# Optimization experiments

Hardware: AMD Instinct MI355X
Metric: run time of the kernel (lower is better)

The kernel has to match this reference:

```python
import jax, jax.numpy as jnp
import numpy as np

N_NODES = 30522
HID = 768
N_EDGES = 488352
B, S = 4, 512
L = 12  # transformer_layers
C = 100  # num classes in pos-neg codebook graph


def setup_inputs() -> dict:
    key = jax.random.key(0)
    ks = jax.random.split(key, 20)
    inp = {}
    inp["word_embs"] = jax.random.normal(ks[0], (N_NODES, HID), dtype=jnp.float32)
    inp["input_ids"] = jax.random.randint(ks[1], (B, S), 0, N_NODES + 1)  # N_NODES = padding row
    inp["class_ids"] = jax.random.randint(ks[2], (B, S), 0, C + 1)
    inp["mask"] = jax.random.randint(ks[3], (B, S, 1), 0, 2).astype(bool)
    inp["co_edge_index"] = jax.random.randint(ks[4], (2, N_EDGES), 0, N_NODES)
    inp["co_edge_weight"] = jax.random.uniform(ks[5], (N_EDGES,), dtype=jnp.float32)
    inp["re_edge_index"] = jax.random.randint(ks[6], (2, N_EDGES), 0, N_NODES)
    inp["re_edge_weight"] = jax.random.uniform(ks[7], (N_EDGES,), dtype=jnp.float32)
    pn_graph = jax.random.uniform(ks[8], (C + 1, N_NODES), dtype=jnp.float32) * 0.01
    inp["pn_graph"] = pn_graph.at[-1].set(0.0)  # padding row of zeros
    sc = 0.02
    inp["co_W"] = jax.random.normal(ks[9], (3, HID, HID), dtype=jnp.float32) * sc
    inp["co_b"] = jnp.zeros((3, HID), jnp.float32)
    inp["re_W"] = jax.random.normal(ks[10], (3, HID, HID), dtype=jnp.float32) * sc
    inp["re_b"] = jnp.zeros((3, HID), jnp.float32)
    inp["pn_W"] = jax.random.normal(ks[11], (HID, HID), dtype=jnp.float32) * sc  # [out,in] 1x1 conv
    inp["pn_b"] = jnp.zeros((HID,), jnp.float32)
    # zero_convs are zero-initialized in the original; use small random so math is non-trivial
    inp["zero_w"] = jax.random.normal(ks[12], (L, HID, HID), dtype=jnp.float32) * sc
    inp["zero_b"] = jnp.zeros((L, HID), jnp.float32)
    inp["zero_w_pos"] = jax.random.normal(ks[13], (L, HID, HID), dtype=jnp.float32) * sc
    inp["zero_b_pos"] = jnp.zeros((L, HID), jnp.float32)
    return inp


def _gcn_layer(x, src, dst, ew, W, b, n):
    # PyG GCNConv: add self-loops (weight 1), symmetric normalization
    deg = jax.ops.segment_sum(ew, dst, num_segments=n) + 1.0
    dinv = jnp.where(deg > 0, jax.lax.rsqrt(deg), 0.0)
    norm = dinv[src] * ew * dinv[dst]  # [E]
    h = x @ W  # [n, H]
    agg = jax.ops.segment_sum(norm[:, None] * h[src], dst, num_segments=n)
    agg = agg + h * (dinv * dinv)[:, None]  # self-loop contribution
    return agg + b


def _gcn_stack(x, edge_index, ew, Ws, bs, ids):
    src, dst = edge_index[0], edge_index[1]
    n = x.shape[0]
    h = x
    acc = None
    for i in range(3):
        h = jax.nn.relu(_gcn_layer(h, src, dst, ew, Ws[i], bs[i], n))
        pad = jnp.concatenate([h, jnp.zeros((1, h.shape[-1]), h.dtype)], axis=0)
        g = pad[ids]  # [B, S, H] gather with padding row
        acc = g if acc is None else acc + g
    return acc / 3.0


def _zero_conv_layers(tok, w, b):
    # 1x1 conv over hidden channels for each of L layers: [B,S,H] x [L,O,H] -> [L,B,S,O]
    return jnp.einsum("bsh,loh->lbso", tok, w) + b[:, None, None, :]


def reference(word_embs, input_ids, class_ids, mask,
              co_edge_index, co_edge_weight, re_edge_index, re_edge_weight,
              pn_graph, co_W, co_b, re_W, re_b, pn_W, pn_b,
              zero_w, zero_b, zero_w_pos, zero_b_pos):
    Bq, Sq = input_ids.shape
    H = word_embs.shape[-1]
    Lq = zero_w.shape[0]
    inv_mask = (~mask).astype(word_embs.dtype)  # [B,S,1]
    zero_pad = jnp.zeros((Lq, Bq, 1, H), word_embs.dtype)

    co = _gcn_stack(word_embs, co_edge_index, co_edge_weight, co_W, co_b, input_ids)  # [B,S,H]
    re = _gcn_stack(word_embs, re_edge_index, re_edge_weight, re_W, re_b, input_ids)

    # NOTE: original uses self.zero_convs (not a separate set) for BOTH co and re
    co_l = _zero_conv_layers(co, zero_w, zero_b) * inv_mask[None]
    re_l = _zero_conv_layers(re, zero_w, zero_b) * inv_mask[None]
    co_l = jnp.concatenate([zero_pad, co_l], axis=2)  # [L,B,S+1,H]
    re_l = jnp.concatenate([zero_pad, re_l], axis=2)

    # PosNegCodebook: 1x1 conv on codebook, then dense-graph matmul, gathered by class
    cb = word_embs @ pn_W.T + pn_b  # [N, H]
    pn = (pn_graph @ cb)[class_ids]  # [B,S,H] (same math as graph[class_ids] @ cb)
    pn_l = _zero_conv_layers(pn, zero_w_pos, zero_b_pos)
    pn_l = jnp.concatenate([zero_pad, pn_l], axis=2)

    return (co_l, re_l, pn_l)
```

## Files before the change

### kernel.cpp

```cpp
#include <hip/hip_runtime.h>
#include <stdint.h>

typedef unsigned int u32;
typedef unsigned short u16;
typedef __attribute__((ext_vector_type(8))) short short8;
typedef __attribute__((ext_vector_type(4))) float f32x4;

#define N_NODESC 30522
#define HIDC 768
#define NEC 488352
#define TOKM 2048
#define LLAY 12
#define NCLS 101
#define M_PAD 30720
#define ZNC (LLAY*HIDC)
#define OUT_SET (LLAY*4*513*HIDC)
#define PN_KCHUNK 512
#define NBLK 120
#define NN1 (N_NODESC+1)
#define G8_LDS 131072

__device__ __forceinline__ float bl(u32 u){ return __uint_as_float(u<<16); }
__device__ __forceinline__ float bh(u32 u){ return __uint_as_float(u & 0xffff0000u); }
__device__ __forceinline__ u32 f2b1(float f){ u32 x=__float_as_uint(f); return (x + 0x7fffu + ((x>>16)&1u))>>16; }
__device__ __forceinline__ u32 pack2(float a, float b){ return f2b1(a) | (f2b1(b)<<16); }

__device__ __forceinline__ void mfma16(f32x4& d, short8 a, short8 b){
  asm volatile("v_mfma_f32_16x16x32_bf16 %0, %1, %2, %0" : "+v"(d) : "v"(a), "v"(b));
}
__device__ __forceinline__ void async16(const void* g, void* l){
  __builtin_amdgcn_global_load_lds((const __attribute__((address_space(1))) u32*)g,
                                   (__attribute__((address_space(3))) u32*)l, 16, 0, 0);
}

__global__ void k_invmask(const void* __restrict__ mask, float* __restrict__ invm){
  __shared__ int s_byte, s_flt;
  int t = threadIdx.x;
  const unsigned char* mb = (const unsigned char*)mask;
  const u32* mw = (const u32*)mask;
  int lb=0, lf=0;
  for(int i=t;i<2048;i+=256) if((i&3)!=0 && mb[i]!=0) lb=1;
  for(int i=t;i<512;i+=256) if(mw[i]==0x3F800000u) lf=1;
  if(t==0){ s_byte=0; s_flt=0; }
  __syncthreads();
  if(lb) s_byte=1;
  if(lf) s_flt=1;
  __syncthreads();
  int mode = s_flt ? 2 : (s_byte ? 1 : 0);
  for(int p=t;p<2048;p+=256){
    int mv = (mode==1) ? (int)mb[p] : (int)(mw[p]!=0u);
    invm[p] = mv ? 0.f : 1.f;
  }
}

__global__ void k_needed(const int* __restrict__ ids, u32* __restrict__ needed){
  int p = blockIdx.x*256 + threadIdx.x;
  if(p < TOKM){ int id = ids[p]; if(id < N_NODESC) needed[id] = 1u; }
}

__global__ void k_need1_init(const u32* __restrict__ needed, u32* __restrict__ need1){
  int v = blockIdx.x*256 + threadIdx.x;
  if(v < N_NODESC){ u32 x = needed[v]; need1[v] = x; need1[N_NODESC + v] = x; }
}
__global__ void k_need_expand(const int* __restrict__ coei, const int* __restrict__ reei,
                              const u32* __restrict__ needed, u32* __restrict__ need1){
  int g = blockIdx.y;
  const int* ei = g ? reei : coei;
  int e = blockIdx.x*256 + threadIdx.x;
  if(e < NEC){
    int d = ei[NEC+e];
    if(needed[d]) need1[(size_t)g*N_NODESC + ei[e]] = 1u;
  }
}

__global__ void k_conv(const float* __restrict__ src, u16* __restrict__ dst, int ndw){
  int i = blockIdx.x*256 + threadIdx.x;
  if(i < ndw) ((u32*)dst)[i] = pack2(src[2*i], src[2*i+1]);
}
__global__ void k_conv_pad(const float* __restrict__ src, u16* __restrict__ dst, int srcRows, int padRows){
  int i = blockIdx.x*256 + threadIdx.x;
  if(i >= padRows*384) return;
  int row = i/384; int c2 = (i - row*384)*2;
  float lo=0.f, hi=0.f;
  if(row < srcRows){ const float* s = src + (size_t)row*HIDC + c2; lo=s[0]; hi=s[1]; }
  ((u32*)dst)[i] = pack2(lo, hi);
}
__global__ void k_pnb(const float* __restrict__ png, u16* __restrict__ pnb){
  int i = blockIdx.x*256 + threadIdx.x;
  if(i >= 128*(M_PAD/2)) return;
  int row = i/(M_PAD/2); int k2 = (i - row*(M_PAD/2))*2;
  float lo=0.f, hi=0.f;
  if(row < NCLS){
    const float* s = png + (size_t)row*N_NODESC;
    if(k2 < N_NODESC) lo = s[k2];
    if(k2+1 < N_NODESC) hi = s[k2+1];
  }
  ((u32*)pnb)[i] = pack2(lo, hi);
}
__global__ void k_transposeW2(const float* __restrict__ coW, const float* __restrict__ reW,
                              u16* __restrict__ Wt2){
  int g = blockIdx.y;
  int i = blockIdx.x*256 + threadIdx.x;
  if(i >= 3*HIDC*384) return;
  const float* W = g ? reW : coW;
  int mat = i/(HIDC*384); int rem = i - mat*HIDC*384;
  int n = rem/384; int kd = rem - n*384;
  const float* Wm = W + (size_t)mat*HIDC*HIDC;
  float lo = Wm[(size_t)(2*kd)*HIDC + n];
  float hi = Wm[(size_t)(2*kd+1)*HIDC + n];
  ((u32*)Wt2)[(size_t)g*3*HIDC*384 + (size_t)mat*HIDC*384 + (size_t)n*384 + kd] = pack2(lo, hi);
}

__global__ void k_degcnt2(const int* __restrict__ coei, const int* __restrict__ reei,
                          const float* __restrict__ coew, const float* __restrict__ reew,
                          float* __restrict__ deg2, int* __restrict__ cnt2){
  int g = blockIdx.y;
  const int* ei = g ? reei : coei;
  const float* ew = g ? reew : coew;
  int e = blockIdx.x*256 + threadIdx.x;
  if(e < NEC){ int d = ei[NEC+e]; atomicAdd(&deg2[(size_t)g*N_NODESC + d], ew[e]); atomicAdd(&cnt2[(size_t)g*N_NODESC + d], 1); }
}
__global__ void k_dinv2(const float* __restrict__ deg2, float* __restrict__ dinvA, float* __restrict__ dinvB){
  int g = blockIdx.y;
  int v = blockIdx.x*256 + threadIdx.x;
  if(v < N_NODESC){
    float d = deg2[(size_t)g*N_NODESC + v] + 1.f;
    dinvA[(size_t)g*N_NODESC + v] = rsqrtf(d);
    dinvB[(size_t)g*N_NODESC + v] = 1.f/d;
  }
}
__global__ void k_scan1(const int* __restrict__ cnt2, int* __restrict__ part2){
  __shared__ int wt[4];
  int g = blockIdx.y, b = blockIdx.x, t = threadIdx.x;
  int lane = t & 63, w = t >> 6;
  int i = b*256 + t;
  int v = (i < N_NODESC) ? cnt2[(size_t)g*N_NODESC + i] : 0;
  int x = v;
  #pragma unroll
  for(int off=1; off<64; off<<=1){ int y = __shfl_up(x, off); if(lane>=off) x += y; }
  if(lane==63) wt[w] = x;
  __syncthreads();
  if(t==0) part2[g*NBLK + b] = wt[0]+wt[1]+wt[2]+wt[3];
}
__global__ void k_scan2(int* __restrict__ part2, int* __restrict__ rp2){
  __shared__ int w0tot;
  int g = blockIdx.x, t = threadIdx.x;
  int lane = t & 63, w = t >> 6;
  int v = (t < NBLK) ? part2[g*NBLK + t] : 0;
  int x = v;
  #pragma unroll
  for(int off=1; off<64; off<<=1){ int y = __shfl_up(x, off); if(lane>=off) x += y; }
  if(w==0 && lane==63) w0tot = x;
  __syncthreads();
  int incl = x + (w ? w0tot : 0);
  int excl = incl - v;
  if(t < NBLK) part2[g*NBLK + t] = excl;
  if(t == 127) rp2[(size_t)g*NN1 + N_NODESC] = incl;
}
__global__ void k_scan3(const int* __restrict__ cnt2, const int* __restrict__ part2,
                        int* __restrict__ rp2, int* __restrict__ cur2){
  __shared__ int wt[4];
  int g = blockIdx.y, b = blockIdx.x, t = threadIdx.x;
  int lane = t & 63, w = t >> 6;
  int i = b*256 + t;
  int v = (i < N_NODESC) ? cnt2[(size_t)g*N_NODESC + i] : 0;
  int x = v;
  #pragma unroll
  for(int off=1; off<64; off<<=1){ int y = __shfl_up(x, off); if(lane>=off) x += y; }
  if(lane==63) wt[w] = x;
  __syncthreads();
  int wpre = 0;
  #pragma unroll
  for(int j=0;j<4;j++) if(j<w) wpre += wt[j];
  int excl = x - v + wpre + part2[g*NBLK + b];
  if(i < N_NODESC){ rp2[(size_t)g*NN1 + i] = excl; cur2[(size_t)g*N_NODESC + i] = excl; }
}
__global__ void k_scatter2(const int* __restrict__ coei, const int* __restrict__ reei,
                           const float* __restrict__ coew, const float* __restrict__ reew,
                           const float* __restrict__ dinvA, int* __restrict__ cur2,
                           float2* __restrict__ emeta){
  int g = blockIdx.y;
  const int* ei = g ? reei : coei;
  const float* ew = g ? reew : coew;
  int e = blockIdx.x*256 + threadIdx.x;
  if(e < NEC){
    int s = ei[e], d = ei[NEC+e];
    int pos = atomicAdd(&cur2[(size_t)g*N_NODESC + d], 1);
    float nrm = dinvA[(size_t)g*N_NODESC + s]*ew[e]*dinvA[(size_t)g*N_NODESC + d];
    emeta[(size_t)g*NEC + pos] = make_float2(__int_as_float(s), nrm);
  }
}

__global__ __launch_bounds__(256)
void k_spmm(const u16* __restrict__ hW, const int* __restrict__ rp,
            const float2* __restrict__ emeta, const float* __restrict__ dinv2,
            const float* __restrict__ bias, u16* __restrict__ hout,
            const u32* __restrict__ needed){
  int v = blockIdx.x*4 + (threadIdx.x>>6);
  if(v >= N_NODESC) return;
  if(needed && !needed[v]) return;
  int lane = threadIdx.x & 63;
  const u32* H = (const u32*)hW;
  float acc[12];
  #pragma unroll
  for(int q=0;q<12;q++) acc[q]=0.f;
  int e0 = rp[v], e1 = rp[v+1];
  int e = e0;
  for(; e+4<=e1; e+=4){
    float2 m0=emeta[e], m1=emeta[e+1], m2=emeta[e+2], m3=emeta[e+3];
    const u32* r0 = H + (size_t)__float_as_int(m0.x)*384 + lane;
    const u32* r1 = H + (size_t)__float_as_int(m1.x)*384 + lane;
    const u32* r2 = H + (size_t)__float_as_int(m2.x)*384 + lane;
    const u32* r3 = H + (size_t)__float_as_int(m3.x)*384 + lane;
    u32 u0[6],u1[6],u2[6],u3[6];
    #pragma unroll
    for(int q=0;q<6;q++){ u0[q]=r0[q*64]; u1[q]=r1[q*64]; u2[q]=r2[q*64]; u3[q]=r3[q*64]; }
    #pragma unroll
    for(int q=0;q<6;q++){
      acc[2*q]   += m0.y*bl(u0[q]) + m1.y*bl(u1[q]) + m2.y*bl(u2[q]) + m3.y*bl(u3[q]);
      acc[2*q+1] += m0.y*bh(u0[q]) + m1.y*bh(u1[q]) + m2.y*bh(u2[q]) + m3.y*bh(u3[q]);
    }
  }
  for(; e<e1; ++e){
    float2 mm = emeta[e];
    const u32* r = H + (size_t)__float_as_int(mm.x)*384 + lane;
    #pragma unroll
    for(int q=0;q<6;q++){ u32 u = r[q*64]; acc[2*q] += mm.y*bl(u); acc[2*q+1] += mm.y*bh(u); }
  }
  { float wgt = dinv2[v];
    const u32* r = H + (size_t)v*384 + lane;
    #pragma unroll
    for(int q=0;q<6;q++){ u32 u = r[q*64]; acc[2*q] += wgt*bl(u); acc[2*q+1] += wgt*bh(u); }
  }
  const float2* B2 = (const float2*)bias;
  u32* O = (u32*)hout + (size_t)v*384 + lane;
  #pragma unroll
  for(int q=0;q<6;q++){
    float2 bb = B2[lane + 64*q];
    float x0 = fmaxf(acc[2*q]+bb.x, 0.f);
    float x1 = fmaxf(acc[2*q+1]+bb.y, 0.f);
    O[q*64] = pack2(x0, x1);
  }
}

__global__ void k_gather(const u16* __restrict__ h, const int* __restrict__ ids,
                         float2* __restrict__ tokf, u16* __restrict__ tokb, int phase){
  int d = blockIdx.x*256 + threadIdx.x;
  if(d >= TOKM*384) return;
  int p = d/384, q = d - p*384;
  int id = ids[p];
  float x0=0.f, x1=0.f;
  if(id < N_NODESC){ u32 u = ((const u32*)h)[(size_t)id*384 + q]; x0 = bl(u)*(1.f/3.f); x1 = bh(u)*(1.f/3.f); }
  float2 cur;
  if(phase==0){ cur.x=x0; cur.y=x1; }
  else { cur = tokf[d]; cur.x += x0; cur.y += x1; }
  if(phase==2) ((u32*)tokb)[d] = pack2(cur.x, cur.y);
  else tokf[d] = cur;
}

__global__ void k_gather_pn(const float* __restrict__ GT, const int* __restrict__ cids, u16* __restrict__ tokb){
  int d = blockIdx.x*256 + threadIdx.x;
  if(d >= TOKM*384) return;
  int p = d/384, q = d - p*384;
  int cid = cids[p];
  float lo = GT[(size_t)(2*q)*128 + cid];
  float hi = GT[(size_t)(2*q+1)*128 + cid];
  ((u32*)tokb)[d] = pack2(lo, hi);
}

__global__ void k_zerocol(float* __restrict__ out){
  int i = blockIdx.x*256 + threadIdx.x;
  if(i >= 3*LLAY*4*HIDC) return;
  int set = i/(LLAY*4*HIDC); int rem = i - set*(LLAY*4*HIDC);
  int l = rem/(4*HIDC); int rem2 = rem - l*(4*HIDC);
  int b = rem2/HIDC; int o = rem2 - b*HIDC;
  out[(size_t)set*OUT_SET + (size_t)(l*4+b)*513*HIDC + o] = 0.f;
}

#define G8_AOFF(b) ((b)*65536)
#define G8_BOFF(b) ((b)*65536 + 32768)

__device__ __forceinline__ void g8_stage(const u16* __restrict__ src, int ldk, int g0, int kt,
                                         char* half_base, int tid){
  const int lane = tid & 63;
  const int csw = ((lane&7) ^ (lane>>3)) << 3;
  const u16* s0 = src + (size_t)(g0 + (tid>>3))*ldk + (kt + csw);
  const u16* s1 = src + (size_t)(g0 + 64 + (tid>>3))*ldk + (kt + csw);
  async16(s0, half_base + (size_t)tid*16);
  async16(s1, half_base + 8192 + (size_t)tid*16);
}

__device__ __forceinline__ void g8_core(const u16* __restrict__ A, const u16* __restrict__ Bt,
                                        int K, int m0, int n0,
                                        f32x4 (&acc)[8][4], char* LDS, int tid){
  const int lane = tid & 63;
  const int wid = tid >> 6;
  const int wr = wid >> 2, wc = wid & 3;
  const int NK = K >> 6;

  g8_stage(Bt, K, n0,      0, LDS + G8_BOFF(0),         tid);
  g8_stage(Bt, K, n0+128,  0, LDS + G8_BOFF(0) + 16384, tid);
  g8_stage(A,  K, m0,      0, LDS + G8_AOFF(0),         tid);
  g8_stage(A,  K, m0+128,  0, LDS + G8_AOFF(0) + 16384, tid);
  g8_stage(Bt, K, n0,     64, LDS + G8_BOFF(1),         tid);
  g8_stage(Bt, K, n0+128, 64, LDS + G8_BOFF(1) + 16384, tid);
  asm volatile("s_waitcnt vmcnt(4)" ::: "memory");
  __builtin_amdgcn_sched_barrier(0);
  __builtin_amdgcn_s_barrier();
  __builtin_amdgcn_sched_barrier(0);

  short8 bf8[8];
  for(int T=0; T<NK; ++T){
    const int buf = T & 1;
    const char* Ab = LDS + G8_AOFF(buf) + wr*16384;
    const char* Bb = LDS + G8_BOFF(buf) + (wc>>1)*16384;
    #pragma unroll
    for(int q=0; q<4; ++q){
      if(q==0){
        #pragma unroll
        for(int n=0;n<4;n++){
          #pragma unroll
          for(int kk=0;kk<2;kk++){
            int row = ((wc&1)<<6) + (n<<4) + (lane&15);
            int cb = ((kk<<6) + ((lane>>4)<<4)) ^ ((lane&7)<<4);
            bf8[n*2+kk] = *(const short8*)(Bb + row*128 + cb);
          }
        }
      }
      short8 af[2][2];
      #pragma unroll
      for(int j=0;j<2;j++){
        #pragma unroll
        for(int kk=0;kk<2;kk++){
          int row = ((2*q+j)<<4) + (lane&15);
          int cb = ((kk<<6) + ((lane>>4)<<4)) ^ ((lane&7)<<4);
          af[j][kk] = *(const short8*)(Ab + row*128 + cb);
        }
      }
      if(q==0 && T+1<NK) g8_stage(A,  K, m0,      (T+1)<<6, LDS + G8_AOFF((T+1)&1),         tid);
      if(q==1 && T+1<NK) g8_stage(A,  K, m0+128,  (T+1)<<6, LDS + G8_AOFF((T+1)&1) + 16384, tid);
      if(q==2 && T+2<NK) g8_stage(Bt, K, n0,      (T+2)<<6, LDS + G8_BOFF(buf),             tid);
      if(q==3 && T+2<NK) g8_stage(Bt, K, n0+128,  (T+2)<<6, LDS + G8_BOFF(buf) + 16384,     tid);
      if(q==3){
        if(T <= NK-3)      asm volatile("s_waitcnt vmcnt(4)" ::: "memory");
        else if(T == NK-2) asm volatile("s_waitcnt vmcnt(0)" ::: "memory");
      }
      __builtin_amdgcn_sched_barrier(0);
      __builtin_amdgcn_s_barrier();
      __builtin_amdgcn_sched_barrier(0);
      __builtin_amdgcn_s_setprio(1);
      #pragma unroll
      for(int j=0;j<2;j++){
        #pragma unroll
        for(int n=0;n<4;n++){
          #pragma unroll
          for(int kk=0;kk<2;kk++) mfma16(acc[2*q+j][n], af[j][kk], bf8[n*2+kk]);
        }
      }
      __builtin_amdgcn_s_setprio(0);
      __builtin_amdgcn_sched_barrier(0);
      __builtin_amdgcn_s_barrier();
      __builtin_amdgcn_sched_barrier(0);
    }
  }
}

__device__ __forceinline__ void g8_split(int ntM, int ntN, int& bm, int& bn){
  int nwg = ntM*ntN;
  int bid = (int)blockIdx.x;
  int wg = (bid & 7)*(nwg>>3) + (bid>>3);
  if(ntN <= ntM){ bm = wg/ntN; bn = wg - bm*ntN; }
  else          { bn = wg/ntM; bm = wg - bn*ntM; }
}

template<int MODE>
__global__ __launch_bounds__(512,2)
void gemm8p_bf16(const u16* __restrict__ A, const u16* __restrict__ Bt,
                 int M, int N, int K,
                 u16* __restrict__ outB, const float* __restrict__ bias){
  extern __shared__ char LDS[];
  const int tid = threadIdx.x;
  const int lane = tid & 63;
  const int wid = tid >> 6;
  const int wr = wid >> 2, wc = wid & 3;
  int bm, bn;
  g8_split(M>>8, N>>8, bm, bn);
  const int m0 = bm << 8, n0 = bn << 8;

  f32x4 acc[8][4];
  f32x4 zv = {0.f,0.f,0.f,0.f};
  #pragma unroll
  for(int m=0;m<8;m++){
    #pragma unroll
    for(int n=0;n<4;n++) acc[m][n] = zv;
  }
  g8_core(A, Bt, K, m0, n0, acc, LDS, tid);

  const int rbase = (lane>>4)<<2;
  const int cbase = lane & 15;
  #pragma unroll
  for(int m=0;m<8;m++){
    int row0 = m0 + (wr<<7) + (m<<4) + rbase;
    #pragma unroll
    for(int n=0;n<4;n++){
      int col = n0 + (wc<<6) + (n<<4) + cbase;
      #pragma unroll
      for(int r=0;r<4;r++){
        float v = acc[m][n][r];
        if(MODE==2) v += bias[row0+r];
        outB[(size_t)(row0+r)*N + col] = (u16)f2b1(v);
      }
    }
  }
}

__global__ __launch_bounds__(512,2)
void gemm8p_zc(const u16* __restrict__ TOKALL, const u16* __restrict__ ZWALL,
               const float* __restrict__ zb, const float* __restrict__ zbp,
               const float* __restrict__ invm, float* __restrict__ out){
  extern __shared__ char LDS[];
  const int set = blockIdx.z;
  const u16* A  = TOKALL + (size_t)set*TOKM*HIDC;
  const u16* Bt = ZWALL + (set==2 ? (size_t)ZNC*HIDC : 0);
  const float* bias = (set==2) ? zbp : zb;
  const bool use_mask = (set != 2);
  float* o = out + (size_t)set*OUT_SET;

  const int tid = threadIdx.x;
  const int lane = tid & 63;
  const int wid = tid >> 6;
  const int wr = wid >> 2, wc = wid & 3;
  int bm, bn;
  g8_split(TOKM>>8, ZNC>>8, bm, bn);
  const int m0 = bm << 8, n0 = bn << 8;

  f32x4 acc[8][4];
  f32x4 zv = {0.f,0.f,0.f,0.f};
  #pragma unroll
  for(int m=0;m<8;m++){
    #pragma unroll
    for(int n=0;n<4;n++) acc[m][n] = zv;
  }
  g8_core(A, Bt, HIDC, m0, n0, acc, LDS, tid);

  const int l = n0 / HIDC;
  const int oc0 = n0 - l*HIDC;
  const int lo = lane & 15, hi = lane >> 4;

  #pragma unroll
  for(int pass=0; pass<2; ++pass){
    __syncthreads();
    if(wr == pass){
      #pragma unroll
      for(int m=0;m<8;m++){
        #pragma unroll
        for(int n=0;n<4;n++){
          int col = (wc<<6) + (n<<4) + lo;
          float badd = bias[n0 + col];
          #pragma unroll
          for(int r=0;r<4;r++){
            int lr = (m<<4) + (hi<<2) + r;
            *(float*)(LDS + (size_t)lr*1024 + ((col<<2) ^ ((lr&7)<<4))) = acc[m][n][r] + badd;
          }
        }
      }
    }
    __syncthreads();
    #pragma unroll
    for(int i=0;i<16;i++){
      int lr = (i<<3) + wid;
      int rr = m0 + (pass<<7) + lr;
      int b = rr >> 9, s = rr & 511;
      f32x4 v = *(const f32x4*)(LDS + (size_t)lr*1024 + ((lane<<4) ^ ((lr&7)<<4)));
      if(use_mask){ float w = invm[rr]; v = v * w; }
      *(f32x4*)(o + (size_t)((l*4+b)*513 + (s+1))*HIDC + oc0 + (lane<<2)) = v;
    }
  }
}

__global__ __launch_bounds__(256,2)
void gemm_splitk(const u16* __restrict__ A, const u16* __restrict__ Bt,
                 int M, int N, int K, float* __restrict__ outF, int kchunk){
  __shared__ u16 As[128*64];
  __shared__ u16 Bs[128*64];
  const int t = threadIdx.x;
  const int lane = t & 63;
  const int w = t >> 6;
  const int wr = w >> 1, wc = w & 1;
  int nchunks = (K + kchunk - 1)/kchunk;
  int bm = (int)blockIdx.x / nchunks;
  int ch = (int)blockIdx.x - bm*nchunks;
  int k0 = ch*kchunk, k1 = k0 + kchunk; if(k1 > K) k1 = K;
  const int m0 = bm << 7, n0 = 0;

  f32x4 zv = {0.f,0.f,0.f,0.f};
  f32x4 acc[4][4];
  #pragma unroll
  for(int m=0;m<4;m++){
    #pragma unroll
    for(int n=0;n<4;n++) acc[m][n] = zv;
  }
  const int srow = t >> 3;
  const int scol = (t & 7) << 3;
  const u16* Ag = A + (size_t)(m0 + srow)*K + scol;
  const u16* Bg = Bt + (size_t)(n0 + srow)*K + scol;
  u16* Al = &As[t*8];
  u16* Bl = &Bs[t*8];

  for(int kt=k0; kt<k1; kt+=64){
    __syncthreads();
    #pragma unroll
    for(int i=0;i<4;i++){
      async16(Ag + (size_t)(i*32)*K + kt, Al + i*2048);
      async16(Bg + (size_t)(i*32)*K + kt, Bl + i*2048);
    }
    __syncthreads();
    #pragma unroll
    for(int kk=0; kk<64; kk+=32){
      const int ko = kk + ((lane>>4)<<3);
      short8 af[4], bfv[4];
      #pragma unroll
      for(int m=0;m<4;m++) af[m] = *(const short8*)&As[((wr<<6)+(m<<4)+(lane&15))*64 + ko];
      #pragma unroll
      for(int n=0;n<4;n++) bfv[n] = *(const short8*)&Bs[((wc<<6)+(n<<4)+(lane&15))*64 + ko];
      #pragma unroll
      for(int m=0;m<4;m++){
        #pragma unroll
        for(int n=0;n<4;n++) mfma16(acc[m][n], af[m], bfv[n]);
      }
    }
  }
  const int rbase = (lane>>4)<<2;
  const int cbase = lane & 15;
  #pragma unroll
  for(int m=0;m<4;m++){
    int row0 = m0 + (wr<<6) + (m<<4) + rbase;
    #pragma unroll
    for(int n=0;n<4;n++){
      int col = n0 + (wc<<6) + (n<<4) + cbase;
      #pragma unroll
      for(int r=0;r<4;r++) atomicAdd(&outF[(size_t)(row0+r)*N + col], acc[m][n][r]);
    }
  }
}

extern "C" void kernel_launch(void* const* d_in, const int* in_sizes, int n_in,
                              void* d_out, int out_size, void* d_ws, size_t ws_size,
                              hipStream_t stream){
  const float* word  = (const float*)d_in[0];
  const int*   ids   = (const int*)d_in[1];
  const int*   cids  = (const int*)d_in[2];
  const void*  mask  = d_in[3];
  const int*   co_ei = (const int*)d_in[4];
  const float* co_ew = (const float*)d_in[5];
  const int*   re_ei = (const int*)d_in[6];
  const float* re_ew = (const float*)d_in[7];
  const float* png   = (const float*)d_in[8];
  const float* co_W  = (const float*)d_in[9];
  const float* co_b  = (const float*)d_in[10];
  const float* re_W  = (const float*)d_in[11];
  const float* re_b  = (const float*)d_in[12];
  const float* pn_W  = (const float*)d_in[13];
  const float* pn_b  = (const float*)d_in[14];
  const float* zw    = (const float*)d_in[15];
  const float* zb    = (const float*)d_in[16];
  const float* zwp   = (const float*)d_in[17];
  const float* zbp   = (const float*)d_in[18];
  float* out = (float*)d_out;

  hipFuncSetAttribute((const void*)gemm8p_bf16<0>, hipFuncAttributeMaxDynamicSharedMemorySize, G8_LDS);
  hipFuncSetAttribute((const void*)gemm8p_bf16<2>, hipFuncAttributeMaxDynamicSharedMemorySize, G8_LDS);
  hipFuncSetAttribute((const void*)gemm8p_zc,      hipFuncAttributeMaxDynamicSharedMemorySize, G8_LDS);

  char* wsb = (char*)d_ws;
  size_t off = 0;
  auto alloc = [&](size_t bytes)->void*{ void* p = wsb + off; off += (bytes + 255) & ~(size_t)255; return p; };
  u16* WORDB = (u16*)alloc((size_t)M_PAD*HIDC*2);
  u16* BUFB  = (u16*)alloc((size_t)M_PAD*HIDC*2);
  u16* BUFX  = (u16*)alloc((size_t)M_PAD*HIDC*2);
  u16* ZWALL = (u16*)alloc((size_t)2*ZNC*HIDC*2);
  u16* WT2   = (u16*)alloc((size_t)2*3*HIDC*HIDC*2);
  u16* PNWB  = (u16*)alloc((size_t)HIDC*HIDC*2);
  u16* PNB   = (u16*)alloc((size_t)128*M_PAD*2);
  u16* TOKALL= (u16*)alloc((size_t)3*TOKM*HIDC*2);
  float2* TOKF = (float2*)alloc((size_t)TOKM*HIDC*4);
  float* GT   = (float*)alloc((size_t)HIDC*128*4);
  float* DEG2 = (float*)alloc((size_t)2*N_NODESC*4);
  int*   CNT2 = (int*)alloc((size_t)2*N_NODESC*4);
  float* DINVA = (float*)alloc((size_t)2*N_NODESC*4);
  float* DINVB = (float*)alloc((size_t)2*N_NODESC*4);
  int*   RP2  = (int*)alloc((size_t)2*NN1*4);
  int*   CUR2 = (int*)alloc((size_t)2*N_NODESC*4);
  int*   PART2= (int*)alloc((size_t)2*NBLK*4);
  float2* EMETA=(float2*)alloc((size_t)2*NEC*8);
  u32*   NEED = (u32*)alloc((size_t)N_NODESC*4);
  u32*   NEED1= (u32*)alloc((size_t)2*N_NODESC*4);
  float* INVM = (float*)alloc((size_t)TOKM*4);
  (void)ws_size; (void)in_sizes; (void)n_in; (void)out_size;

  const int GD_TOK = (TOKM*384 + 255)/256;
  const int GD_E   = (NEC + 255)/256;
  const int GD_N   = (N_NODESC + 255)/256;
  const int SPMM_GD  = (N_NODESC + 3)/4;
  const int PN_NCHUNKS = M_PAD/PN_KCHUNK;
  const int G_PN  = (HIDC/128)*PN_NCHUNKS;
  const int G8_GCN = (M_PAD/256)*(HIDC/256);
  const int G8_CBT = (HIDC/256)*(M_PAD/256);
  const int G8_ZC  = (TOKM/256)*(ZNC/256);

  hipMemsetAsync(NEED, 0, (size_t)N_NODESC*4, stream);
  hipMemsetAsync(DEG2, 0, (size_t)2*N_NODESC*4, stream);
  hipMemsetAsync(CNT2, 0, (size_t)2*N_NODESC*4, stream);
  k_invmask<<<1,256,0,stream>>>(mask, INVM);
  k_needed<<<(TOKM+255)/256,256,0,stream>>>(ids, NEED);
  k_need1_init<<<GD_N,256,0,stream>>>(NEED, NEED1);
  k_need_expand<<<dim3(GD_E,2),256,0,stream>>>(co_ei, re_ei, NEED, NEED1);
  k_conv<<<(HIDC*HIDC/2 + 255)/256,256,0,stream>>>(pn_W, PNWB, HIDC*HIDC/2);
  k_conv<<<(ZNC*HIDC/2 + 255)/256,256,0,stream>>>(zw, ZWALL, ZNC*HIDC/2);
  k_conv<<<(ZNC*HIDC/2 + 255)/256,256,0,stream>>>(zwp, ZWALL + (size_t)ZNC*HIDC, ZNC*HIDC/2);
  k_conv_pad<<<(M_PAD*384 + 255)/256,256,0,stream>>>(word, WORDB, N_NODESC, M_PAD);
  k_transposeW2<<<dim3((3*HIDC*384 + 255)/256, 2),256,0,stream>>>(co_W, re_W, WT2);

  k_degcnt2<<<dim3(GD_E,2),256,0,stream>>>(co_ei, re_ei, co_ew, re_ew, DEG2, CNT2);
  k_dinv2<<<dim3(GD_N,2),256,0,stream>>>(DEG2, DINVA, DINVB);
  k_scan1<<<dim3(NBLK,2),256,0,stream>>>(CNT2, PART2);
  k_scan2<<<2,128,0,stream>>>(PART2, RP2);
  k_scan3<<<dim3(NBLK,2),256,0,stream>>>(CNT2, PART2, RP2, CUR2);
  k_scatter2<<<dim3(GD_E,2),256,0,stream>>>(co_ei, re_ei, co_ew, re_ew, DINVA, CUR2, EMETA);

  gemm8p_bf16<2><<<G8_CBT,512,G8_LDS,stream>>>(PNWB, WORDB, HIDC, M_PAD, HIDC, BUFX, pn_b);
  k_pnb<<<(128*(M_PAD/2) + 255)/256,256,0,stream>>>(png, PNB);
  hipMemsetAsync(GT, 0, (size_t)HIDC*128*4, stream);
  gemm_splitk<<<G_PN,256,0,stream>>>(BUFX, PNB, HIDC, 128, M_PAD, GT, PN_KCHUNK);
  k_gather_pn<<<GD_TOK,256,0,stream>>>(GT, cids, TOKALL + (size_t)2*TOKM*HIDC);

  auto run_graph = [&](int g, const float* bf, u16* tokb){
    const int* rp = RP2 + (size_t)g*NN1;
    const float2* em = EMETA + (size_t)g*NEC;
    const float* di2 = DINVB + (size_t)g*N_NODESC;
    const u16* X = WORDB;
    for(int i=0;i<3;i++){
      gemm8p_bf16<0><<<G8_GCN,512,G8_LDS,stream>>>(X, WT2 + ((size_t)g*3 + i)*HIDC*HIDC,
                                                   M_PAD, HIDC, HIDC, BUFB, nullptr);
      const u32* flt = (i==2) ? NEED : (i==1 ? NEED1 + (size_t)g*N_NODESC : nullptr);
      k_spmm<<<SPMM_GD,256,0,stream>>>(BUFB, rp, em, di2, bf + i*HIDC, BUFX, flt);
      k_gather<<<GD_TOK,256,0,stream>>>(BUFX, ids, TOKF, tokb, i);
      X = BUFX;
    }
  };
  run_graph(0, co_b, TOKALL);
  run_graph(1, re_b, TOKALL + (size_t)TOKM*HIDC);

  dim3 zgrid(G8_ZC, 1, 3);
  gemm8p_zc<<<zgrid,512,G8_LDS,stream>>>(TOKALL, ZWALL, zb, zbp, INVM, out);
  k_zerocol<<<(3*LLAY*4*HIDC + 255)/256,256,0,stream>>>(out);
}
```

Before: 1.224 ms.

## Switch bf16 GEMMs from 256x256 8-wave tiles to 128x128 4-wave tiles

Replaces the 256x256, 512-thread GEMM core with a 128x128, 256-thread core using 64 KB of LDS. It restructures the pipeline: a whole k-tile is loaded into registers up front, MFMAs are split into two halves, and the prefetch of tile T+2 is issued between them. The zero-conv epilogue is redone in a single pass with float2 stores. The aim is more workgroups for load balance and occupancy on the small-N GEMMs (N=768), at the cost of lower arithmetic intensity per tile and more global traffic.

```diff
diff --git a/kernel.cpp b/kernel.cpp
--- a/kernel.cpp
+++ b/kernel.cpp
@@ -18,7 +18,7 @@
 #define PN_KCHUNK 512
 #define NBLK 120
 #define NN1 (N_NODESC+1)
-#define G8_LDS 131072
+#define G4_LDS 65536
 
 __device__ __forceinline__ float bl(u32 u){ return __uint_as_float(u<<16); }
 __device__ __forceinline__ float bh(u32 u){ return __uint_as_float(u & 0xffff0000u); }
@@ -277,95 +277,86 @@
   out[(size_t)set*OUT_SET + (size_t)(l*4+b)*513*HIDC + o] = 0.f;
 }
 
-#define G8_AOFF(b) ((b)*65536)
-#define G8_BOFF(b) ((b)*65536 + 32768)
-
-__device__ __forceinline__ void g8_stage(const u16* __restrict__ src, int ldk, int g0, int kt,
-                                         char* half_base, int tid){
+#define G4_ABUF(b) ((b)*32768)
+#define G4_BBUF(b) ((b)*32768 + 16384)
+
+__device__ __forceinline__ void g4_stage(const u16* __restrict__ src, int ldk, int g0, int kt,
+                                         char* base, int tid){
   const int lane = tid & 63;
   const int csw = ((lane&7) ^ (lane>>3)) << 3;
-  const u16* s0 = src + (size_t)(g0 + (tid>>3))*ldk + (kt + csw);
-  const u16* s1 = src + (size_t)(g0 + 64 + (tid>>3))*ldk + (kt + csw);
-  async16(s0, half_base + (size_t)tid*16);
-  async16(s1, half_base + 8192 + (size_t)tid*16);
-}
-
-__device__ __forceinline__ void g8_core(const u16* __restrict__ A, const u16* __restrict__ Bt,
+  const int r = tid >> 3;
+  #pragma unroll
+  for(int h=0; h<4; ++h)
+    async16(src + (size_t)(g0 + h*32 + r)*ldk + (kt + csw), base + h*4096 + (size_t)tid*16);
+}
+
+__device__ __forceinline__ void g4_core(const u16* __restrict__ A, const u16* __restrict__ Bt,
                                         int K, int m0, int n0,
-                                        f32x4 (&acc)[8][4], char* LDS, int tid){
+                                        f32x4 (&acc)[4][4], char* LDS, int tid){
   const int lane = tid & 63;
   const int wid = tid >> 6;
-  const int wr = wid >> 2, wc = wid & 3;
+  const int wr = wid >> 1, wc = wid & 1;
   const int NK = K >> 6;
 
-  g8_stage(Bt, K, n0,      0, LDS + G8_BOFF(0),         tid);
-  g8_stage(Bt, K, n0+128,  0, LDS + G8_BOFF(0) + 16384, tid);
-  g8_stage(A,  K, m0,      0, LDS + G8_AOFF(0),         tid);
-  g8_stage(A,  K, m0+128,  0, LDS + G8_AOFF(0) + 16384, tid);
-  g8_stage(Bt, K, n0,     64, LDS + G8_BOFF(1),         tid);
-  g8_stage(Bt, K, n0+128, 64, LDS + G8_BOFF(1) + 16384, tid);
-  asm volatile("s_waitcnt vmcnt(4)" ::: "memory");
-  __builtin_amdgcn_sched_barrier(0);
-  __builtin_amdgcn_s_barrier();
-  __builtin_amdgcn_sched_barrier(0);
-
-  short8 bf8[8];
+  g4_stage(A,  K, m0,  0, LDS + G4_ABUF(0), tid);
+  g4_stage(Bt, K, n0,  0, LDS + G4_BBUF(0), tid);
+  g4_stage(A,  K, m0, 64, LDS + G4_ABUF(1), tid);
+  g4_stage(Bt, K, n0, 64, LDS + G4_BBUF(1), tid);
+
+  short8 af[4][2], bf[4][2];
   for(int T=0; T<NK; ++T){
     const int buf = T & 1;
-    const char* Ab = LDS + G8_AOFF(buf) + wr*16384;
-    const char* Bb = LDS + G8_BOFF(buf) + (wc>>1)*16384;
-    #pragma unroll
-    for(int q=0; q<4; ++q){
-      if(q==0){
+    const char* Ab = LDS + G4_ABUF(buf) + wr*8192;
+    const char* Bb = LDS + G4_BBUF(buf) + wc*8192;
+    if(T+1 < NK) asm volatile("s_waitcnt vmcnt(8)" ::: "memory");
+    else         asm volatile("s_waitcnt vmcnt(0)" ::: "memory");
+    __builtin_amdgcn_sched_barrier(0);
+    __builtin_amdgcn_s_barrier();
+    __builtin_amdgcn_sched_barrier(0);
+    #pragma unroll
+    for(int m=0;m<4;m++){
+      #pragma unroll
+      for(int kk=0;kk<2;kk++){
+        int row = (m<<4) + (lane&15);
+        int cb = ((kk<<6) + ((lane>>4)<<4)) ^ ((lane&7)<<4);
+        af[m][kk] = *(const short8*)(Ab + row*128 + cb);
+        bf[m][kk] = *(const short8*)(Bb + row*128 + cb);
+      }
+    }
+    asm volatile("s_waitcnt lgkmcnt(0)" ::: "memory");
+    __builtin_amdgcn_sched_barrier(0);
+    __builtin_amdgcn_s_setprio(1);
+    #pragma unroll
+    for(int m=0;m<2;m++){
+      #pragma unroll
+      for(int n=0;n<4;n++){
         #pragma unroll
-        for(int n=0;n<4;n++){
-          #pragma unroll
-          for(int kk=0;kk<2;kk++){
-            int row = ((wc&1)<<6) + (n<<4) + (lane&15);
-            int cb = ((kk<<6) + ((lane>>4)<<4)) ^ ((lane&7)<<4);
-            bf8[n*2+kk] = *(const short8*)(Bb + row*128 + cb);
-          }
-        }
+        for(int kk=0;kk<2;kk++) mfma16(acc[m][n], af[m][kk], bf[n][kk]);
       }
-      short8 af[2][2];
-      #pragma unroll
-      for(int j=0;j<2;j++){
+    }
+    __builtin_amdgcn_s_setprio(0);
+    __builtin_amdgcn_sched_barrier(0);
+    __builtin_amdgcn_s_barrier();
+    __builtin_amdgcn_sched_barrier(0);
+    if(T+2 < NK){
+      g4_stage(A,  K, m0, (T+2)<<6, LDS + G4_ABUF(buf), tid);
+      g4_stage(Bt, K, n0, (T+2)<<6, LDS + G4_BBUF(buf), tid);
+    }
+    __builtin_amdgcn_s_setprio(1);
+    #pragma unroll
+    for(int m=2;m<4;m++){
+      #pragma unroll
+      for(int n=0;n<4;n++){
         #pragma unroll
-        for(int kk=0;kk<2;kk++){
-          int row = ((2*q+j)<<4) + (lane&15);
-          int cb = ((kk<<6) + ((lane>>4)<<4)) ^ ((lane&7)<<4);
-          af[j][kk] = *(const short8*)(Ab + row*128 + cb);
-        }
+        for(int kk=0;kk<2;kk++) mfma16(acc[m][n], af[m][kk], bf[n][kk]);
       }
-      if(q==0 && T+1<NK) g8_stage(A,  K, m0,      (T+1)<<6, LDS + G8_AOFF((T+1)&1),         tid);
-      if(q==1 && T+1<NK) g8_stage(A,  K, m0+128,  (T+1)<<6, LDS + G8_AOFF((T+1)&1) + 16384, tid);
-      if(q==2 && T+2<NK) g8_stage(Bt, K, n0,      (T+2)<<6, LDS + G8_BOFF(buf),             tid);
-      if(q==3 && T+2<NK) g8_stage(Bt, K, n0+128,  (T+2)<<6, LDS + G8_BOFF(buf) + 16384,     tid);
-      if(q==3){
-        if(T <= NK-3)      asm volatile("s_waitcnt vmcnt(4)" ::: "memory");
-        else if(T == NK-2) asm volatile("s_waitcnt vmcnt(0)" ::: "memory");
-      }
-      __builtin_amdgcn_sched_barrier(0);
-      __builtin_amdgcn_s_barrier();
-      __builtin_amdgcn_sched_barrier(0);
-      __builtin_amdgcn_s_setprio(1);
-      #pragma unroll
-      for(int j=0;j<2;j++){
-        #pragma unroll
-        for(int n=0;n<4;n++){
-          #pragma unroll
-          for(int kk=0;kk<2;kk++) mfma16(acc[2*q+j][n], af[j][kk], bf8[n*2+kk]);
-        }
-      }
-      __builtin_amdgcn_s_setprio(0);
-      __builtin_amdgcn_sched_barrier(0);
-      __builtin_amdgcn_s_barrier();
-      __builtin_amdgcn_sched_barrier(0);
-    }
-  }
-}
-
-__device__ __forceinline__ void g8_split(int ntM, int ntN, int& bm, int& bn){
+    }
+    __builtin_amdgcn_s_setprio(0);
+    __builtin_amdgcn_sched_barrier(0);
+  }
+}
+
+__device__ __forceinline__ void g_split(int ntM, int ntN, int& bm, int& bn){
   int nwg = ntM*ntN;
   int bid = (int)blockIdx.x;
   int wg = (bid & 7)*(nwg>>3) + (bid>>3);
@@ -374,33 +365,33 @@
 }
 
 template<int MODE>
-__global__ __launch_bounds__(512,2)
-void gemm8p_bf16(const u16* __restrict__ A, const u16* __restrict__ Bt,
+__global__ __launch_bounds__(256,2)
+void gemm4p_bf16(const u16* __restrict__ A, const u16* __restrict__ Bt,
                  int M, int N, int K,
                  u16* __restrict__ outB, const float* __restrict__ bias){
   extern __shared__ char LDS[];
   const int tid = threadIdx.x;
   const int lane = tid & 63;
   const int wid = tid >> 6;
-  const int wr = wid >> 2, wc = wid & 3;
+  const int wr = wid >> 1, wc = wid & 1;
   int bm, bn;
-  g8_split(M>>8, N>>8, bm, bn);
-  const int m0 = bm << 8, n0 = bn << 8;
-
-  f32x4 acc[8][4];
+  g_split(M>>7, N>>7, bm, bn);
+  const int m0 = bm << 7, n0 = bn << 7;
+
+  f32x4 acc[4][4];
   f32x4 zv = {0.f,0.f,0.f,0.f};
   #pragma unroll
-  for(int m=0;m<8;m++){
+  for(int m=0;m<4;m++){
     #pragma unroll
     for(int n=0;n<4;n++) acc[m][n] = zv;
   }
-  g8_core(A, Bt, K, m0, n0, acc, LDS, tid);
+  g4_core(A, Bt, K, m0, n0, acc, LDS, tid);
 
   const int rbase = (lane>>4)<<2;
   const int cbase = lane & 15;
   #pragma unroll
-  for(int m=0;m<8;m++){
-    int row0 = m0 + (wr<<7) + (m<<4) + rbase;
+  for(int m=0;m<4;m++){
+    int row0 = m0 + (wr<<6) + (m<<4) + rbase;
     #pragma unroll
     for(int n=0;n<4;n++){
       int col = n0 + (wc<<6) + (n<<4) + cbase;
@@ -414,8 +405,8 @@
   }
 }
 
-__global__ __launch_bounds__(512,2)
-void gemm8p_zc(const u16* __restrict__ TOKALL, const u16* __restrict__ ZWALL,
+__global__ __launch_bounds__(256,2)
+void gemm4p_zc(const u16* __restrict__ TOKALL, const u16* __restrict__ ZWALL,
                const float* __restrict__ zb, const float* __restrict__ zbp,
                const float* __restrict__ invm, float* __restrict__ out){
   extern __shared__ char LDS[];
@@ -429,52 +420,47 @@
   const int tid = threadIdx.x;
   const int lane = tid & 63;
   const int wid = tid >> 6;
-  const int wr = wid >> 2, wc = wid & 3;
+  const int wr = wid >> 1, wc = wid & 1;
   int bm, bn;
-  g8_split(TOKM>>8, ZNC>>8, bm, bn);
-  const int m0 = bm << 8, n0 = bn << 8;
-
-  f32x4 acc[8][4];
+  g_split(TOKM>>7, ZNC>>7, bm, bn);
+  const int m0 = bm << 7, n0 = bn << 7;
+
+  f32x4 acc[4][4];
   f32x4 zv = {0.f,0.f,0.f,0.f};
   #pragma unroll
-  for(int m=0;m<8;m++){
+  for(int m=0;m<4;m++){
     #pragma unroll
     for(int n=0;n<4;n++) acc[m][n] = zv;
   }
-  g8_core(A, Bt, HIDC, m0, n0, acc, LDS, tid);
+  g4_core(A, Bt, HIDC, m0, n0, acc, LDS, tid);
 
   const int l = n0 / HIDC;
   const int oc0 = n0 - l*HIDC;
   const int lo = lane & 15, hi = lane >> 4;
 
-  #pragma unroll
-  for(int pass=0; pass<2; ++pass){
-    __syncthreads();
-    if(wr == pass){
-      #pragma unroll
-      for(int m=0;m<8;m++){
-        #pragma unroll
-        for(int n=0;n<4;n++){
-          int col = (wc<<6) + (n<<4) + lo;
-          float badd = bias[n0 + col];
-          #pragma unroll
-          for(int r=0;r<4;r++){
-            int lr = (m<<4) + (hi<<2) + r;
-            *(float*)(LDS + (size_t)lr*1024 + ((col<<2) ^ ((lr&7)<<4))) = acc[m][n][r] + badd;
-          }
-        }
+  __syncthreads();
+  #pragma unroll
+  for(int m=0;m<4;m++){
+    #pragma unroll
+    for(int n=0;n<4;n++){
+      int c = (wc<<6) + (n<<4) + lo;
+      float badd = bias[n0 + c];
+      #pragma unroll
+      for(int r=0;r<4;r++){
+        int lr = (wr<<6) + (m<<4) + (hi<<2) + r;
+        *(float*)(LDS + (size_t)lr*512 + (((c<<2) ^ ((lr&7)<<4)))) = acc[m][n][r] + badd;
       }
     }
-    __syncthreads();
-    #pragma unroll
-    for(int i=0;i<16;i++){
-      int lr = (i<<3) + wid;
-      int rr = m0 + (pass<<7) + lr;
-      int b = rr >> 9, s = rr & 511;
-      f32x4 v = *(const f32x4*)(LDS + (size_t)lr*1024 + ((lane<<4) ^ ((lr&7)<<4)));
-      if(use_mask){ float w = invm[rr]; v = v * w; }
-      *(f32x4*)(o + (size_t)((l*4+b)*513 + (s+1))*HIDC + oc0 + (lane<<2)) = v;
-    }
+  }
+  __syncthreads();
+  #pragma unroll
+  for(int i=0;i<32;i++){
+    int lr = (i<<2) + wid;
+    int rr = m0 + lr;
+    int b = rr >> 9, s = rr & 511;
+    float2 v = *(const float2*)(LDS + (size_t)lr*512 + ((lane<<3) ^ ((lr&7)<<4)));
+    if(use_mask){ float w = invm[rr]; v.x *= w; v.y *= w; }
+    *(float2*)(o + (size_t)((l*4+b)*513 + (s+1))*HIDC + oc0 + (lane<<1)) = v;
   }
 }
 
@@ -568,9 +554,9 @@
   const float* zbp   = (const float*)d_in[18];
   float* out = (float*)d_out;
 
-  hipFuncSetAttribute((const void*)gemm8p_bf16<0>, hipFuncAttributeMaxDynamicSharedMemorySize, G8_LDS);
-  hipFuncSetAttribute((const void*)gemm8p_bf16<2>, hipFuncAttributeMaxDynamicSharedMemorySize, G8_LDS);
-  hipFuncSetAttribute((const void*)gemm8p_zc,      hipFuncAttributeMaxDynamicSharedMemorySize, G8_LDS);
+  hipFuncSetAttribute((const void*)gemm4p_bf16<0>, hipFuncAttributeMaxDynamicSharedMemorySize, G4_LDS);
+  hipFuncSetAttribute((const void*)gemm4p_bf16<2>, hipFuncAttributeMaxDynamicSharedMemorySize, G4_LDS);
+  hipFuncSetAttribute((const void*)gemm4p_zc,      hipFuncAttributeMaxDynamicSharedMemorySize, G4_LDS);
 
   char* wsb = (char*)d_ws;
   size_t off = 0;
@@ -604,9 +590,9 @@
   const int SPMM_GD  = (N_NODESC + 3)/4;
   const int PN_NCHUNKS = M_PAD/PN_KCHUNK;
   const int G_PN  = (HIDC/128)*PN_NCHUNKS;
-  const int G8_GCN = (M_PAD/256)*(HIDC/256);
-  const int G8_CBT = (HIDC/256)*(M_PAD/256);
-  const int G8_ZC  = (TOKM/256)*(ZNC/256);
+  const int G4_GCN = (M_PAD/128)*(HIDC/128);
+  const int G4_CBT = (HIDC/128)*(M_PAD/128);
+  const int G4_ZC  = (TOKM/128)*(ZNC/128);
 
   hipMemsetAsync(NEED, 0, (size_t)N_NODESC*4, stream);
   hipMemsetAsync(DEG2, 0, (size_t)2*N_NODESC*4, stream);
@@ -628,7 +614,7 @@
   k_scan3<<<dim3(NBLK,2),256,0,stream>>>(CNT2, PART2, RP2, CUR2);
   k_scatter2<<<dim3(GD_E,2),256,0,stream>>>(co_ei, re_ei, co_ew, re_ew, DINVA, CUR2, EMETA);
 
-  gemm8p_bf16<2><<<G8_CBT,512,G8_LDS,stream>>>(PNWB, WORDB, HIDC, M_PAD, HIDC, BUFX, pn_b);
+  gemm4p_bf16<2><<<G4_CBT,256,G4_LDS,stream>>>(PNWB, WORDB, HIDC, M_PAD, HIDC, BUFX, pn_b);
   k_pnb<<<(128*(M_PAD/2) + 255)/256,256,0,stream>>>(png, PNB);
   hipMemsetAsync(GT, 0, (size_t)HIDC*128*4, stream);
   gemm_splitk<<<G_PN,256,0,stream>>>(BUFX, PNB, HIDC, 128, M_PAD, GT, PN_KCHUNK);
@@ -640,7 +626,7 @@
     const float* di2 = DINVB + (size_t)g*N_NODESC;
     const u16* X = WORDB;
     for(int i=0;i<3;i++){
-      gemm8p_bf16<0><<<G8_GCN,512,G8_LDS,stream>>>(X, WT2 + ((size_t)g*3 + i)*HIDC*HIDC,
+      gemm4p_bf16<0><<<G4_GCN,256,G4_LDS,stream>>>(X, WT2 + ((size_t)g*3 + i)*HIDC*HIDC,
                                                    M_PAD, HIDC, HIDC, BUFB, nullptr);
       const u32* flt = (i==2) ? NEED : (i==1 ? NEED1 + (size_t)g*N_NODESC : nullptr);
       k_spmm<<<SPMM_GD,256,0,stream>>>(BUFB, rp, em, di2, bf + i*HIDC, BUFX, flt);
@@ -651,7 +637,7 @@
   run_graph(0, co_b, TOKALL);
   run_graph(1, re_b, TOKALL + (size_t)TOKM*HIDC);
 
-  dim3 zgrid(G8_ZC, 1, 3);
-  gemm8p_zc<<<zgrid,512,G8_LDS,stream>>>(TOKALL, ZWALL, zb, zbp, INVM, out);
+  dim3 zgrid(G4_ZC, 1, 3);
+  gemm4p_zc<<<zgrid,256,G4_LDS,stream>>>(TOKALL, ZWALL, zb, zbp, INVM, out);
   k_zerocol<<<(3*LLAY*4*HIDC + 255)/256,256,0,stream>>>(out);
 }
```

New measurement: 1.168 ms. 4.5% less time.

## Replace 256x256 GEMM tiles with 128x128 four-wave kernel for GCN and codebook

Applied to the files above, without the earlier changes.

Adds a new 128x128-tile, 256-thread bf16 GEMM with double-buffered async LDS staging and uses it for the GCN feature transforms and the codebook 1x1 conv in place of the 256x256, 512-thread kernel. Smaller tiles give four times as many workgroups (1440 instead of 360 for M=30720, N=768), which should fill the CUs better and cut tail imbalance. The cost is lower arithmetic intensity per tile, so there is more global and LDS traffic per FLOP. The zero-conv GEMM keeps the large-tile kernel.

```diff
diff --git a/kernel.cpp b/kernel.cpp
--- a/kernel.cpp
+++ b/kernel.cpp
@@ -18,6 +18,7 @@
 #define PN_KCHUNK 512
 #define NBLK 120
 #define NN1 (N_NODESC+1)
+#define G4_LDS 65536
 #define G8_LDS 131072
 
 __device__ __forceinline__ float bl(u32 u){ return __uint_as_float(u<<16); }
@@ -277,6 +278,14 @@
   out[(size_t)set*OUT_SET + (size_t)(l*4+b)*513*HIDC + o] = 0.f;
 }
 
+__device__ __forceinline__ void g_split(int ntM, int ntN, int& bm, int& bn){
+  int nwg = ntM*ntN;
+  int bid = (int)blockIdx.x;
+  int wg = (bid & 7)*(nwg>>3) + (bid>>3);
+  if(ntN <= ntM){ bm = wg/ntN; bn = wg - bm*ntN; }
+  else          { bn = wg/ntM; bm = wg - bn*ntM; }
+}
+
 #define G8_AOFF(b) ((b)*65536)
 #define G8_BOFF(b) ((b)*65536 + 32768)
 
@@ -365,55 +374,6 @@
   }
 }
 
-__device__ __forceinline__ void g8_split(int ntM, int ntN, int& bm, int& bn){
-  int nwg = ntM*ntN;
-  int bid = (int)blockIdx.x;
-  int wg = (bid & 7)*(nwg>>3) + (bid>>3);
-  if(ntN <= ntM){ bm = wg/ntN; bn = wg - bm*ntN; }
-  else          { bn = wg/ntM; bm = wg - bn*ntM; }
-}
-
-template<int MODE>
-__global__ __launch_bounds__(512,2)
-void gemm8p_bf16(const u16* __restrict__ A, const u16* __restrict__ Bt,
-                 int M, int N, int K,
-                 u16* __restrict__ outB, const float* __restrict__ bias){
-  extern __shared__ char LDS[];
-  const int tid = threadIdx.x;
-  const int lane = tid & 63;
-  const int wid = tid >> 6;
-  const int wr = wid >> 2, wc = wid & 3;
-  int bm, bn;
-  g8_split(M>>8, N>>8, bm, bn);
-  const int m0 = bm << 8, n0 = bn << 8;
-
-  f32x4 acc[8][4];
-  f32x4 zv = {0.f,0.f,0.f,0.f};
-  #pragma unroll
-  for(int m=0;m<8;m++){
-    #pragma unroll
-    for(int n=0;n<4;n++) acc[m][n] = zv;
-  }
-  g8_core(A, Bt, K, m0, n0, acc, LDS, tid);
-
-  const int rbase = (lane>>4)<<2;
-  const int cbase = lane & 15;
-  #pragma unroll
-  for(int m=0;m<8;m++){
-    int row0 = m0 + (wr<<7) + (m<<4) + rbase;
-    #pragma unroll
-    for(int n=0;n<4;n++){
-      int col = n0 + (wc<<6) + (n<<4) + cbase;
-      #pragma unroll
-      for(int r=0;r<4;r++){
-        float v = acc[m][n][r];
-        if(MODE==2) v += bias[row0+r];
-        outB[(size_t)(row0+r)*N + col] = (u16)f2b1(v);
-      }
-    }
-  }
-}
-
 __global__ __launch_bounds__(512,2)
 void gemm8p_zc(const u16* __restrict__ TOKALL, const u16* __restrict__ ZWALL,
                const float* __restrict__ zb, const float* __restrict__ zbp,
@@ -431,7 +391,7 @@
   const int wid = tid >> 6;
   const int wr = wid >> 2, wc = wid & 3;
   int bm, bn;
-  g8_split(TOKM>>8, ZNC>>8, bm, bn);
+  g_split(TOKM>>8, ZNC>>8, bm, bn);
   const int m0 = bm << 8, n0 = bn << 8;
 
   f32x4 acc[8][4];
@@ -474,6 +434,126 @@
       f32x4 v = *(const f32x4*)(LDS + (size_t)lr*1024 + ((lane<<4) ^ ((lr&7)<<4)));
       if(use_mask){ float w = invm[rr]; v = v * w; }
       *(f32x4*)(o + (size_t)((l*4+b)*513 + (s+1))*HIDC + oc0 + (lane<<2)) = v;
+    }
+  }
+}
+
+#define G4_ABUF(b) ((b)*32768)
+#define G4_BBUF(b) ((b)*32768 + 16384)
+
+__device__ __forceinline__ void g4_stage(const u16* __restrict__ src, int ldk, int g0, int kt,
+                                         char* base, int tid){
+  const int lane = tid & 63;
+  const int csw = ((lane&7) ^ (lane>>3)) << 3;
+  const int r = tid >> 3;
+  #pragma unroll
+  for(int h=0; h<4; ++h)
+    async16(src + (size_t)(g0 + h*32 + r)*ldk + (kt + csw), base + h*4096 + (size_t)tid*16);
+}
+
+__device__ __forceinline__ void g4_core(const u16* __restrict__ A, const u16* __restrict__ Bt,
+                                        int K, int m0, int n0,
+                                        f32x4 (&acc)[4][4], char* LDS, int tid){
+  const int lane = tid & 63;
+  const int wid = tid >> 6;
+  const int wr = wid >> 1, wc = wid & 1;
+  const int NK = K >> 6;
+
+  g4_stage(A,  K, m0,  0, LDS + G4_ABUF(0), tid);
+  g4_stage(Bt, K, n0,  0, LDS + G4_BBUF(0), tid);
+  g4_stage(A,  K, m0, 64, LDS + G4_ABUF(1), tid);
+  g4_stage(Bt, K, n0, 64, LDS + G4_BBUF(1), tid);
+
+  short8 af[4][2], bf[4][2];
+  for(int T=0; T<NK; ++T){
+    const int buf = T & 1;
+    const char* Ab = LDS + G4_ABUF(buf) + wr*8192;
+    const char* Bb = LDS + G4_BBUF(buf) + wc*8192;
+    if(T+1 < NK) asm volatile("s_waitcnt vmcnt(8)" ::: "memory");
+    else         asm volatile("s_waitcnt vmcnt(0)" ::: "memory");
+    __builtin_amdgcn_sched_barrier(0);
+    __builtin_amdgcn_s_barrier();
+    __builtin_amdgcn_sched_barrier(0);
+    #pragma unroll
+    for(int m=0;m<4;m++){
+      #pragma unroll
+      for(int kk=0;kk<2;kk++){
+        int row = (m<<4) + (lane&15);
+        int cb = ((kk<<6) + ((lane>>4)<<4)) ^ ((lane&7)<<4);
+        af[m][kk] = *(const short8*)(Ab + row*128 + cb);
+        bf[m][kk] = *(const short8*)(Bb + row*128 + cb);
+      }
+    }
+    asm volatile("s_waitcnt lgkmcnt(0)" ::: "memory");
+    __builtin_amdgcn_sched_barrier(0);
+    __builtin_amdgcn_s_setprio(1);
+    #pragma unroll
+    for(int m=0;m<2;m++){
+      #pragma unroll
+      for(int n=0;n<4;n++){
+        #pragma unroll
+        for(int kk=0;kk<2;kk++) mfma16(acc[m][n], af[m][kk], bf[n][kk]);
+      }
+    }
+    __builtin_amdgcn_s_setprio(0);
+    __builtin_amdgcn_sched_barrier(0);
+    __builtin_amdgcn_s_barrier();
+    __builtin_amdgcn_sched_barrier(0);
+    if(T+2 < NK){
+      g4_stage(A,  K, m0, (T+2)<<6, LDS + G4_ABUF(buf), tid);
+      g4_stage(Bt, K, n0, (T+2)<<6, LDS + G4_BBUF(buf), tid);
+    }
+    __builtin_amdgcn_s_setprio(1);
+    #pragma unroll
+    for(int m=2;m<4;m++){
+      #pragma unroll
+      for(int n=0;n<4;n++){
+        #pragma unroll
+        for(int kk=0;kk<2;kk++) mfma16(acc[m][n], af[m][kk], bf[n][kk]);
+      }
+    }
+    __builtin_amdgcn_s_setprio(0);
+    __builtin_amdgcn_sched_barrier(0);
+  }
+}
+
+template<int MODE>
+__global__ __launch_bounds__(256,2)
+void gemm4p_bf16(const u16* __restrict__ A, const u16* __restrict__ Bt,
+                 int M, int N, int K,
+                 u16* __restrict__ outB, const float* __restrict__ bias){
+  extern __shared__ char LDS[];
+  const int tid = threadIdx.x;
+  const int lane = tid & 63;
+  const int wid = tid >> 6;
+  const int wr = wid >> 1, wc = wid & 1;
+  int bm, bn;
+  g_split(M>>7, N>>7, bm, bn);
+  const int m0 = bm << 7, n0 = bn << 7;
+
+  f32x4 acc[4][4];
+  f32x4 zv = {0.f,0.f,0.f,0.f};
+  #pragma unroll
+  for(int m=0;m<4;m++){
+    #pragma unroll
+    for(int n=0;n<4;n++) acc[m][n] = zv;
+  }
+  g4_core(A, Bt, K, m0, n0, acc, LDS, tid);
+
+  const int rbase = (lane>>4)<<2;
+  const int cbase = lane & 15;
+  #pragma unroll
+  for(int m=0;m<4;m++){
+    int row0 = m0 + (wr<<6) + (m<<4) + rbase;
+    #pragma unroll
+    for(int n=0;n<4;n++){
+      int col = n0 + (wc<<6) + (n<<4) + cbase;
+      #pragma unroll
+      for(int r=0;r<4;r++){
+        float v = acc[m][n][r];
+        if(MODE==2) v += bias[row0+r];
+        outB[(size_t)(row0+r)*N + col] = (u16)f2b1(v);
+      }
     }
   }
 }
@@ -568,8 +648,8 @@
   const float* zbp   = (const float*)d_in[18];
   float* out = (float*)d_out;
 
-  hipFuncSetAttribute((const void*)gemm8p_bf16<0>, hipFuncAttributeMaxDynamicSharedMemorySize, G8_LDS);
-  hipFuncSetAttribute((const void*)gemm8p_bf16<2>, hipFuncAttributeMaxDynamicSharedMemorySize, G8_LDS);
+  hipFuncSetAttribute((const void*)gemm4p_bf16<0>, hipFuncAttributeMaxDynamicSharedMemorySize, G4_LDS);
+  hipFuncSetAttribute((const void*)gemm4p_bf16<2>, hipFuncAttributeMaxDynamicSharedMemorySize, G4_LDS);
   hipFuncSetAttribute((const void*)gemm8p_zc,      hipFuncAttributeMaxDynamicSharedMemorySize, G8_LDS);
 
   char* wsb = (char*)d_ws;
@@ -604,8 +684,8 @@
   const int SPMM_GD  = (N_NODESC + 3)/4;
   const int PN_NCHUNKS = M_PAD/PN_KCHUNK;
   const int G_PN  = (HIDC/128)*PN_NCHUNKS;
-  const int G8_GCN = (M_PAD/256)*(HIDC/256);
-  const int G8_CBT = (HIDC/256)*(M_PAD/256);
+  const int G4_GCN = (M_PAD/128)*(HIDC/128);
+  const int G4_CBT = (HIDC/128)*(M_PAD/128);
   const int G8_ZC  = (TOKM/256)*(ZNC/256);
 
   hipMemsetAsync(NEED, 0, (size_t)N_NODESC*4, stream);
@@ -628,7 +708,7 @@
   k_scan3<<<dim3(NBLK,2),256,0,stream>>>(CNT2, PART2, RP2, CUR2);
   k_scatter2<<<dim3(GD_E,2),256,0,stream>>>(co_ei, re_ei, co_ew, re_ew, DINVA, CUR2, EMETA);
 
-  gemm8p_bf16<2><<<G8_CBT,512,G8_LDS,stream>>>(PNWB, WORDB, HIDC, M_PAD, HIDC, BUFX, pn_b);
+  gemm4p_bf16<2><<<G4_CBT,256,G4_LDS,stream>>>(PNWB, WORDB, HIDC, M_PAD, HIDC, BUFX, pn_b);
   k_pnb<<<(128*(M_PAD/2) + 255)/256,256,0,stream>>>(png, PNB);
   hipMemsetAsync(GT, 0, (size_t)HIDC*128*4, stream);
   gemm_splitk<<<G_PN,256,0,stream>>>(BUFX, PNB, HIDC, 128, M_PAD, GT, PN_KCHUNK);
@@ -640,7 +720,7 @@
     const float* di2 = DINVB + (size_t)g*N_NODESC;
     const u16* X = WORDB;
     for(int i=0;i<3;i++){
-      gemm8p_bf16<0><<<G8_GCN,512,G8_LDS,stream>>>(X, WT2 + ((size_t)g*3 + i)*HIDC*HIDC,
+      gemm4p_bf16<0><<<G4_GCN,256,G4_LDS,stream>>>(X, WT2 + ((size_t)g*3 + i)*HIDC*HIDC,
                                                    M_PAD, HIDC, HIDC, BUFB, nullptr);
       const u32* flt = (i==2) ? NEED : (i==1 ? NEED1 + (size_t)g*N_NODESC : nullptr);
       k_spmm<<<SPMM_GD,256,0,stream>>>(BUFB, rp, em, di2, bf + i*HIDC, BUFX, flt);
```

Result: faster. 1.140 ms (-6.9%).
